# Optimization experiments

Measured on AMD Instinct MI355X. Metric: run time of the kernel, lower is better.

## Reference

```python
import jax, jax.numpy as jnp
import numpy as np

N_NODES = 50000
N_EDGES = 800000
N_GRAPHS = 512
IN_CH = 64
HID = 64
NEG_SLOPE = 0.2  # PyG GATConv default


def leaky_relu(x):
    return jnp.where(x >= 0, x, NEG_SLOPE * x)


def gat_conv(x, src, dst, W, a_src, a_dst, bias):
    # x: [N, in]; src/dst: [E] (self-loops already included)
    h = x @ W                                   # [N, hid]
    # per-edge attention logits (heads=1)
    alpha_s = h @ a_src                         # [N]
    alpha_d = h @ a_dst                         # [N]
    logits = leaky_relu(alpha_s[src] + alpha_d[dst])   # [E]
    # segment softmax over destination nodes
    seg_max = jax.ops.segment_max(logits, dst, num_segments=N_NODES)
    seg_max = jnp.where(jnp.isfinite(seg_max), seg_max, 0.0)
    ex = jnp.exp(logits - seg_max[dst])
    denom = jax.ops.segment_sum(ex, dst, num_segments=N_NODES)
    alpha = ex / jnp.maximum(denom[dst], 1e-16)
    # scatter-weighted aggregation of source features
    out = jax.ops.segment_sum(alpha[:, None] * h[src], dst, num_segments=N_NODES)
    return out + bias


def setup_inputs() -> dict:
    key = jax.random.key(0)
    ks = jax.random.split(key, 12)
    x = jax.random.normal(ks[0], (N_NODES, IN_CH), dtype=jnp.float32)
    edge_index = jax.random.randint(ks[1], (2, N_EDGES), 0, N_NODES, dtype=jnp.int64)
    batch = jnp.sort(jax.random.randint(ks[2], (N_NODES,), 0, N_GRAPHS, dtype=jnp.int64))
    s1 = 1.0 / np.sqrt(IN_CH)
    s2 = 1.0 / np.sqrt(HID)
    W1 = jax.random.normal(ks[3], (IN_CH, HID), dtype=jnp.float32) * s1
    a_src1 = jax.random.normal(ks[4], (HID,), dtype=jnp.float32) * s2
    a_dst1 = jax.random.normal(ks[5], (HID,), dtype=jnp.float32) * s2
    b1 = jnp.zeros((HID,), dtype=jnp.float32)
    W2 = jax.random.normal(ks[6], (HID, HID), dtype=jnp.float32) * s2
    a_src2 = jax.random.normal(ks[7], (HID,), dtype=jnp.float32) * s2
    a_dst2 = jax.random.normal(ks[8], (HID,), dtype=jnp.float32) * s2
    b2 = jnp.zeros((HID,), dtype=jnp.float32)
    return {"x": x, "edge_index": edge_index, "batch": batch,
            "W1": W1, "a_src1": a_src1, "a_dst1": a_dst1, "b1": b1,
            "W2": W2, "a_src2": a_src2, "a_dst2": a_dst2, "b2": b2}


def reference(x, edge_index, batch, W1, a_src1, a_dst1, b1, W2, a_src2, a_dst2, b2):
    # add self-loops (PyG GATConv default add_self_loops=True)
    loops = jnp.arange(N_NODES, dtype=edge_index.dtype)
    src = jnp.concatenate([edge_index[0], loops])
    dst = jnp.concatenate([edge_index[1], loops])
    h = jax.nn.elu(gat_conv(x, src, dst, W1, a_src1, a_dst1, b1))
    h = jax.nn.elu(gat_conv(h, src, dst, W2, a_src2, a_dst2, b2))
    # global mean pool per graph
    sums = jax.ops.segment_sum(h, batch, num_segments=N_GRAPHS)        # [G, hid]
    cnt = jax.ops.segment_sum(jnp.ones((N_NODES,), h.dtype), batch, num_segments=N_GRAPHS)
    return sums / jnp.maximum(cnt, 1.0)[:, None]
```

## Files before the change

### kernel.cpp

```cpp
#include <hip/hip_runtime.h>
#include <hip/hip_bf16.h>
#include <math.h>

#define N_NODES_C 50000
#define N_EDGES_C 800000
#define E_TOT_C   (N_EDGES_C + N_NODES_C)
#define N_GRAPHS_C 512
#define CH 64
#define NBUCK 391
#define NB_BUCK 256
#define BCAP 3328
#define TRF_NODES 64
#define NB_TRF ((N_NODES_C + TRF_NODES - 1) / TRF_NODES)

__device__ __forceinline__ float wave_reduce_sum(float v) {
#pragma unroll
    for (int m = 32; m >= 1; m >>= 1) v += __shfl_xor(v, m, 64);
    return v;
}


__global__ __launch_bounds__(256) void prelim_kernel(
    const int* __restrict__ batch, int* __restrict__ gstart, int* __restrict__ bucket_cnt,
    const float* __restrict__ W1, const float* __restrict__ as1, const float* __restrict__ ad1,
    const float* __restrict__ W2, const float* __restrict__ as2, const float* __restrict__ ad2,
    float* __restrict__ wa)
{
    int blk = blockIdx.x, t = threadIdx.x;
    if (blk >= 196) {
        if (t < 64) {
            const float* W  = (blk == 196) ? W1  : W2;
            const float* As = (blk == 196) ? as1 : as2;
            const float* Ad = (blk == 196) ? ad1 : ad2;
            float ss = 0.f, dd = 0.f;
#pragma unroll 8
            for (int c = 0; c < 64; ++c) {
                float w = W[t * 64 + c];
                ss = fmaf(w, As[c], ss);
                dd = fmaf(w, Ad[c], dd);
            }
            float* o = wa + ((blk == 196) ? 0 : 128);
            o[t] = ss; o[64 + t] = dd;
        }
        return;
    }
    int i = blk * 256 + t;
    if (i < NBUCK) bucket_cnt[i] = 0;
    if (i >= N_NODES_C) return;
    int bcur = batch[i];
    int bprev = (i > 0) ? batch[i - 1] : -1;
    for (int g = bprev + 1; g <= bcur; ++g) gstart[g] = i;
    if (i == N_NODES_C - 1)
        for (int g = bcur + 1; g <= N_GRAPHS_C; ++g) gstart[g] = N_NODES_C;
}


struct TrfSmem {
    float Wl[64][64];
    __align__(16) float xs[64][68];
    float wsv[64], wdv[64];
};
struct BuildSmem { int cnt[NBUCK]; int lbase[NBUCK]; };
union __align__(16) FusedSmem { TrfSmem t; BuildSmem b; };


__device__ __forceinline__ void build_body(
    BuildSmem& sm, int blk, const int* __restrict__ ei,
    int* __restrict__ bucket_cnt, unsigned int* __restrict__ buck_edges)
{
    int t = threadIdx.x;
    for (int i = t; i < NBUCK; i += 256) sm.cnt[i] = 0;
    __syncthreads();
    const int CHUNK = (E_TOT_C + NB_BUCK - 1) / NB_BUCK;
    int beg = blk * CHUNK, end = min(beg + CHUNK, E_TOT_C);
    for (int e = beg + t; e < end; e += 256) {
        int d = (e < N_EDGES_C) ? ei[N_EDGES_C + e] : (e - N_EDGES_C);
        atomicAdd(&sm.cnt[d >> 7], 1);
    }
    __syncthreads();
    for (int b = t; b < NBUCK; b += 256) {
        int c = sm.cnt[b];
        sm.lbase[b] = (c > 0) ? atomicAdd(&bucket_cnt[b], c) : 0;
        sm.cnt[b] = 0;
    }
    __syncthreads();
    for (int e = beg + t; e < end; e += 256) {
        int s_, d_;
        if (e < N_EDGES_C) { s_ = ei[e]; d_ = ei[N_EDGES_C + e]; }
        else               { s_ = d_ = e - N_EDGES_C; }
        int b = d_ >> 7;
        int pos = sm.lbase[b] + atomicAdd(&sm.cnt[b], 1);
        buck_edges[b * BCAP + pos] = ((unsigned)(d_ & 127) << 16) | (unsigned)s_;
    }
}


__device__ __forceinline__ void transform_body(
    TrfSmem& sm, int bb,
    const float* __restrict__ xin, const float* __restrict__ W,
    const float* __restrict__ wa,
    __hip_bfloat16* __restrict__ hout, float* __restrict__ as_out,
    float* __restrict__ ad_out)
{
    int t = threadIdx.x;
    const float4* W4 = (const float4*)W;
    float4* Wl4 = (float4*)&sm.Wl[0][0];
    for (int i = t; i < 1024; i += 256) Wl4[i] = W4[i];
    if (t < 64) sm.wsv[t] = wa[t];
    else if (t < 128) sm.wdv[t - 64] = wa[t];
    int n0 = bb * TRF_NODES;
    int nn = min(TRF_NODES, N_NODES_C - n0);
    if (nn < TRF_NODES) {
        for (int idx = t; idx < 64 * TRF_NODES; idx += 256) {
            int k = idx >> 6, row = idx & 63;
            if (row >= nn) sm.xs[k][row] = 0.f;
        }
    }
    for (int idx = t; idx < nn * 16; idx += 256) {
        int row = idx >> 4, f4 = idx & 15;
        float4 v = *reinterpret_cast<const float4*>(xin + (size_t)(n0 + row) * CH + f4 * 4);
        sm.xs[f4 * 4 + 0][row] = v.x;
        sm.xs[f4 * 4 + 1][row] = v.y;
        sm.xs[f4 * 4 + 2][row] = v.z;
        sm.xs[f4 * 4 + 3][row] = v.w;
    }
    __syncthreads();
    int w = t >> 6, c = t & 63, lane = t & 63;
    int r0 = w * 16;
    float acc[16];
#pragma unroll
    for (int i = 0; i < 16; ++i) acc[i] = 0.f;
#pragma unroll 8
    for (int k = 0; k < 64; ++k) {
        float wl = sm.Wl[k][c];
        const float4* xp = reinterpret_cast<const float4*>(&sm.xs[k][r0]);
        float4 xa = xp[0], xb = xp[1], xc = xp[2], xd = xp[3];
        acc[0]  = fmaf(xa.x, wl, acc[0]);  acc[1]  = fmaf(xa.y, wl, acc[1]);
        acc[2]  = fmaf(xa.z, wl, acc[2]);  acc[3]  = fmaf(xa.w, wl, acc[3]);
        acc[4]  = fmaf(xb.x, wl, acc[4]);  acc[5]  = fmaf(xb.y, wl, acc[5]);
        acc[6]  = fmaf(xb.z, wl, acc[6]);  acc[7]  = fmaf(xb.w, wl, acc[7]);
        acc[8]  = fmaf(xc.x, wl, acc[8]);  acc[9]  = fmaf(xc.y, wl, acc[9]);
        acc[10] = fmaf(xc.z, wl, acc[10]); acc[11] = fmaf(xc.w, wl, acc[11]);
        acc[12] = fmaf(xd.x, wl, acc[12]); acc[13] = fmaf(xd.y, wl, acc[13]);
        acc[14] = fmaf(xd.z, wl, acc[14]); acc[15] = fmaf(xd.w, wl, acc[15]);
    }
    size_t hb = (size_t)(n0 + r0) * CH + c;
#pragma unroll
    for (int i = 0; i < 16; ++i)
        if (r0 + i < nn) hout[hb + (size_t)i * CH] = __float2bfloat16(acc[i]);
    int kb = lane & 3;
    int rloc = r0 + (lane >> 2);
    float ps = 0.f, pd = 0.f;
#pragma unroll
    for (int j = 0; j < 16; ++j) {
        int k = kb + 4 * j;
        float xv = sm.xs[k][rloc];
        ps = fmaf(xv, sm.wsv[k], ps);
        pd = fmaf(xv, sm.wdv[k], pd);
    }
    ps += __shfl_xor(ps, 1, 64); ps += __shfl_xor(ps, 2, 64);
    pd += __shfl_xor(pd, 1, 64); pd += __shfl_xor(pd, 2, 64);
    if (kb == 0 && rloc < nn) {
        as_out[n0 + rloc] = ps;
        ad_out[n0 + rloc] = pd;
    }
}


__global__ __launch_bounds__(256) void fused_build_trf(
    const int* __restrict__ ei, int* __restrict__ bucket_cnt,
    unsigned int* __restrict__ buck_edges,
    const float* __restrict__ xin, const float* __restrict__ W,
    const float* __restrict__ wa,
    __hip_bfloat16* __restrict__ hout, float* __restrict__ as_out,
    float* __restrict__ ad_out)
{
    __shared__ FusedSmem sm;
    if (blockIdx.x < NB_BUCK)
        build_body(sm.b, blockIdx.x, ei, bucket_cnt, buck_edges);
    else
        transform_body(sm.t, blockIdx.x - NB_BUCK, xin, W, wa, hout, as_out, ad_out);
}

__global__ __launch_bounds__(256) void transform_kernel(
    const float* __restrict__ xin, const float* __restrict__ W,
    const float* __restrict__ wa,
    __hip_bfloat16* __restrict__ hout, float* __restrict__ as_out,
    float* __restrict__ ad_out)
{
    __shared__ TrfSmem sm;
    transform_body(sm, blockIdx.x, xin, W, wa, hout, as_out, ad_out);
}


__global__ __launch_bounds__(512) void bucket_to_csr(const unsigned int* __restrict__ buck_edges,
                                                     const int* __restrict__ bucket_cnt,
                                                     unsigned short* __restrict__ csr_src,
                                                     unsigned int* __restrict__ row_ptr) {
    __shared__ unsigned int ebuf[BCAP];
    __shared__ unsigned short sbuf[BCAP];
    __shared__ int deg[128], off[128], cur[128];
    __shared__ int wsum;
    int bb = blockIdx.x, t = threadIdx.x;
    int base = bb * BCAP;
    int size = min(bucket_cnt[bb], BCAP);
    int node0 = bb << 7;
    int nnodes = min(128, N_NODES_C - node0);
    for (int i = t; i < size; i += 512) ebuf[i] = buck_edges[base + i];
    if (t < 128) deg[t] = 0;
    __syncthreads();
    for (int i = t; i < size; i += 512) atomicAdd(&deg[(ebuf[i] >> 16) & 127], 1);
    __syncthreads();
    int myscan = 0;
    if (t < 128) {
        int l = t & 63;
        int s = deg[t];
#pragma unroll
        for (int o = 1; o < 64; o <<= 1) {
            int u = __shfl_up(s, o, 64);
            if (l >= o) s += u;
        }
        myscan = s;
        if (t == 63) wsum = s;
    }
    __syncthreads();
    if (t < 128) {
        int add = (t >= 64) ? wsum : 0;
        off[t] = myscan + add - deg[t];
        cur[t] = 0;
    }
    __syncthreads();
    for (int i = t; i < size; i += 512) {
        unsigned pk = ebuf[i];
        int l = (pk >> 16) & 127;
        int p = atomicAdd(&cur[l], 1);
        sbuf[off[l] + p] = (unsigned short)(pk & 0xFFFFu);
    }
    __syncthreads();
    for (int i = t; i < size; i += 512) csr_src[base + i] = sbuf[i];
    if (t < nnodes)
        row_ptr[node0 + t] = ((unsigned)(base + off[t]) << 8) | (unsigned)min(deg[t], 255);
}


__global__ __launch_bounds__(256) void aggregate_kernel(
    const __hip_bfloat16* __restrict__ h, const float* __restrict__ as,
    const float* __restrict__ ad, const float* __restrict__ bias,
    const unsigned int* __restrict__ row_ptr, const unsigned short* __restrict__ csr_src,
    float* __restrict__ out)
{
    int t = threadIdx.x;
    int w = t >> 6, lane = t & 63;
    int n = blockIdx.x * 4 + w;
    unsigned rp = row_ptr[n];
    int beg = (int)(rp >> 8);
    int deg = (int)(rp & 255u);
    float adn = ad[n];
    if (deg <= 64) {
        int sub = lane >> 3;
        int cg  = (lane & 7) << 3;
        int ch  = cg | sub;
        float bch = bias[ch];
        int s_reg = (int)csr_src[beg + min(lane, deg - 1)];
        float ex = 0.f;
        if (lane < deg) {
            float v = as[s_reg] + adn;
            v = (v >= 0.f) ? v : 0.2f * v;
            ex = __expf(v);
        }
        float ssum = wave_reduce_sum(ex);
        float inv = 1.f / fmaxf(ssum, 1e-16f);
        float a0 = 0.f, a1 = 0.f, a2 = 0.f, a3 = 0.f;
        float a4 = 0.f, a5 = 0.f, a6 = 0.f, a7 = 0.f;
        int full = deg >> 4, rem = deg & 15;
        for (int j = 0; j < full; ++j) {
            int e1 = j * 16 + sub;
            int e2 = e1 + 8;
            int   s1 = __shfl(s_reg, e1, 64);
            int   s2 = __shfl(s_reg, e2, 64);
            float w1 = __shfl(ex, e1, 64);
            float w2 = __shfl(ex, e2, 64);
            uint4 u1 = *reinterpret_cast<const uint4*>(h + (size_t)s1 * CH + cg);
            uint4 u2 = *reinterpret_cast<const uint4*>(h + (size_t)s2 * CH + cg);
            a0 = fmaf(w1, __uint_as_float(u1.x << 16), a0);
            a1 = fmaf(w1, __uint_as_float(u1.x & 0xFFFF0000u), a1);
            a2 = fmaf(w1, __uint_as_float(u1.y << 16), a2);
            a3 = fmaf(w1, __uint_as_float(u1.y & 0xFFFF0000u), a3);
            a4 = fmaf(w1, __uint_as_float(u1.z << 16), a4);
            a5 = fmaf(w1, __uint_as_float(u1.z & 0xFFFF0000u), a5);
            a6 = fmaf(w1, __uint_as_float(u1.w << 16), a6);
            a7 = fmaf(w1, __uint_as_float(u1.w & 0xFFFF0000u), a7);
            a0 = fmaf(w2, __uint_as_float(u2.x << 16), a0);
            a1 = fmaf(w2, __uint_as_float(u2.x & 0xFFFF0000u), a1);
            a2 = fmaf(w2, __uint_as_float(u2.y << 16), a2);
            a3 = fmaf(w2, __uint_as_float(u2.y & 0xFFFF0000u), a3);
            a4 = fmaf(w2, __uint_as_float(u2.z << 16), a4);
            a5 = fmaf(w2, __uint_as_float(u2.z & 0xFFFF0000u), a5);
            a6 = fmaf(w2, __uint_as_float(u2.w << 16), a6);
            a7 = fmaf(w2, __uint_as_float(u2.w & 0xFFFF0000u), a7);
        }
        if (rem) {
            int e1 = full * 16 + sub;
            int   s1 = __shfl(s_reg, e1, 64);
            float w1 = __shfl(ex, e1, 64);
            uint4 u1 = make_uint4(0, 0, 0, 0);
            if (e1 < deg) u1 = *reinterpret_cast<const uint4*>(h + (size_t)s1 * CH + cg);
            a0 = fmaf(w1, __uint_as_float(u1.x << 16), a0);
            a1 = fmaf(w1, __uint_as_float(u1.x & 0xFFFF0000u), a1);
            a2 = fmaf(w1, __uint_as_float(u1.y << 16), a2);
            a3 = fmaf(w1, __uint_as_float(u1.y & 0xFFFF0000u), a3);
            a4 = fmaf(w1, __uint_as_float(u1.z << 16), a4);
            a5 = fmaf(w1, __uint_as_float(u1.z & 0xFFFF0000u), a5);
            a6 = fmaf(w1, __uint_as_float(u1.w << 16), a6);
            a7 = fmaf(w1, __uint_as_float(u1.w & 0xFFFF0000u), a7);
            if (rem > 8) {
                int e2 = e1 + 8;
                int   s2 = __shfl(s_reg, e2, 64);
                float w2 = __shfl(ex, e2, 64);
                uint4 u2 = make_uint4(0, 0, 0, 0);
                if (e2 < deg) u2 = *reinterpret_cast<const uint4*>(h + (size_t)s2 * CH + cg);
                a0 = fmaf(w2, __uint_as_float(u2.x << 16), a0);
                a1 = fmaf(w2, __uint_as_float(u2.x & 0xFFFF0000u), a1);
                a2 = fmaf(w2, __uint_as_float(u2.y << 16), a2);
                a3 = fmaf(w2, __uint_as_float(u2.y & 0xFFFF0000u), a3);
                a4 = fmaf(w2, __uint_as_float(u2.z << 16), a4);
                a5 = fmaf(w2, __uint_as_float(u2.z & 0xFFFF0000u), a5);
                a6 = fmaf(w2, __uint_as_float(u2.w << 16), a6);
                a7 = fmaf(w2, __uint_as_float(u2.w & 0xFFFF0000u), a7);
            }
        }
        bool hi5 = (lane & 32) != 0;
        float t0 = __shfl_xor(hi5 ? a0 : a4, 32, 64);
        float t1 = __shfl_xor(hi5 ? a1 : a5, 32, 64);
        float t2 = __shfl_xor(hi5 ? a2 : a6, 32, 64);
        float t3 = __shfl_xor(hi5 ? a3 : a7, 32, 64);
        float b0 = (hi5 ? a4 : a0) + t0;
        float b1 = (hi5 ? a5 : a1) + t1;
        float b2 = (hi5 ? a6 : a2) + t2;
        float b3 = (hi5 ? a7 : a3) + t3;
        bool hi4 = (lane & 16) != 0;
        float u0 = __shfl_xor(hi4 ? b0 : b2, 16, 64);
        float u1s = __shfl_xor(hi4 ? b1 : b3, 16, 64);
        float c0 = (hi4 ? b2 : b0) + u0;
        float c1 = (hi4 ? b3 : b1) + u1s;
        bool hi3 = (lane & 8) != 0;
        float v1 = __shfl_xor(hi3 ? c0 : c1, 8, 64);
        float r  = (hi3 ? c1 : c0) + v1;
        float v = r * inv + bch;
        v = (v > 0.f) ? v : __expf(v) - 1.f;
        out[(size_t)n * CH + ch] = v;
    } else {
        int end = beg + deg;
        float ssum = 0.f;
        for (int i = beg + lane; i < end; i += 64) {
            float v = as[csr_src[i]] + adn;
            v = (v >= 0.f) ? v : 0.2f * v;
            ssum += __expf(v);
        }
        ssum = wave_reduce_sum(ssum);
        float inv = 1.f / fmaxf(ssum, 1e-16f);
        float acc = 0.f;
        for (int i = beg; i < end; ++i) {
            int s = csr_src[i];
            float v = as[s] + adn;
            v = (v >= 0.f) ? v : 0.2f * v;
            float ww = __expf(v);
            acc = fmaf(ww, __bfloat162float(h[(size_t)s * CH + lane]), acc);
        }
        acc = acc * inv + bias[lane];
        out[(size_t)n * CH + lane] = (acc > 0.f) ? acc : __expf(acc) - 1.f;
    }
}


__global__ __launch_bounds__(256) void pool_kernel(
    const float* __restrict__ h, const int* __restrict__ gstart,
    float* __restrict__ out)
{
    __shared__ float red[4][64];
    int g = blockIdx.x;
    int t = threadIdx.x, w = t >> 6, lane = t & 63;
    int beg = gstart[g], end = gstart[g + 1];
    float acc = 0.f;
    for (int n = beg + w; n < end; n += 4) acc += h[n * CH + lane];
    red[w][lane] = acc;
    __syncthreads();
    if (w == 0) {
        float v = red[0][lane] + red[1][lane] + red[2][lane] + red[3][lane];
        float c = (float)(end - beg);
        out[g * CH + lane] = v / fmaxf(c, 1.f);
    }
}


extern "C" void kernel_launch(void* const* d_in, const int* in_sizes, int n_in,
                              void* d_out, int out_size, void* d_ws, size_t ws_size,
                              hipStream_t stream)
{
    const float* x   = (const float*)d_in[0];
    const int*   ei  = (const int*)d_in[1];
    const int*   bat = (const int*)d_in[2];
    const float* W1  = (const float*)d_in[3];
    const float* as1 = (const float*)d_in[4];
    const float* ad1 = (const float*)d_in[5];
    const float* b1  = (const float*)d_in[6];
    const float* W2  = (const float*)d_in[7];
    const float* as2 = (const float*)d_in[8];
    const float* ad2 = (const float*)d_in[9];
    const float* b2  = (const float*)d_in[10];
    float* out = (float*)d_out;

    char* ws = (char*)d_ws;
    size_t off = 0;
    auto alloc = [&](size_t bytes) -> void* {
        void* p = ws + off;
        off += (bytes + 255) & ~size_t(255);
        return p;
    };
    __hip_bfloat16* hbuf = (__hip_bfloat16*)alloc(sizeof(__hip_bfloat16) * N_NODES_C * CH);
    float* obuf    = (float*)alloc(sizeof(float) * N_NODES_C * CH);
    float* alpha_s = (float*)alloc(sizeof(float) * N_NODES_C);
    float* alpha_d = (float*)alloc(sizeof(float) * N_NODES_C);
    int*   bucket_cnt = (int*)alloc(sizeof(int) * NBUCK);
    unsigned int* buck_edges = (unsigned int*)alloc(sizeof(unsigned) * NBUCK * BCAP);
    unsigned short* csr_src  = (unsigned short*)alloc(sizeof(unsigned short) * NBUCK * BCAP);
    unsigned int* row_ptr    = (unsigned int*)alloc(sizeof(unsigned) * N_NODES_C);
    int*   gstart  = (int*)alloc(sizeof(int) * (N_GRAPHS_C + 1));
    float* wa      = (float*)alloc(sizeof(float) * 256);

    const int NB_AGG = N_NODES_C / 4;

    prelim_kernel<<<198, 256, 0, stream>>>(bat, gstart, bucket_cnt,
                                           W1, as1, ad1, W2, as2, ad2, wa);
    fused_build_trf<<<NB_BUCK + NB_TRF, 256, 0, stream>>>(ei, bucket_cnt, buck_edges,
                                                          x, W1, wa, hbuf, alpha_s, alpha_d);
    bucket_to_csr<<<NBUCK, 512, 0, stream>>>(buck_edges, bucket_cnt, csr_src, row_ptr);

    aggregate_kernel<<<NB_AGG, 256, 0, stream>>>(hbuf, alpha_s, alpha_d, b1,
                                                 row_ptr, csr_src, obuf);
    transform_kernel<<<NB_TRF, 256, 0, stream>>>(obuf, W2, wa + 128, hbuf, alpha_s, alpha_d);
    aggregate_kernel<<<NB_AGG, 256, 0, stream>>>(hbuf, alpha_s, alpha_d, b2,
                                                 row_ptr, csr_src, obuf);

    pool_kernel<<<N_GRAPHS_C, 256, 0, stream>>>(obuf, gstart, out);
}
```

Measured before the change: 180.2 us.

## Remove prelim kernel, fold its work into other kernels, add small-degree aggregate path

Result: faster. 175.0 us (-2.9%).

```diff
diff --git a/kernel.cpp b/kernel.cpp
--- a/kernel.cpp
+++ b/kernel.cpp
@@ -19,44 +19,20 @@
     return v;
 }
 
-
-__global__ __launch_bounds__(256) void prelim_kernel(
-    const int* __restrict__ batch, int* __restrict__ gstart, int* __restrict__ bucket_cnt,
-    const float* __restrict__ W1, const float* __restrict__ as1, const float* __restrict__ ad1,
-    const float* __restrict__ W2, const float* __restrict__ as2, const float* __restrict__ ad2,
-    float* __restrict__ wa)
-{
-    int blk = blockIdx.x, t = threadIdx.x;
-    if (blk >= 196) {
-        if (t < 64) {
-            const float* W  = (blk == 196) ? W1  : W2;
-            const float* As = (blk == 196) ? as1 : as2;
-            const float* Ad = (blk == 196) ? ad1 : ad2;
-            float ss = 0.f, dd = 0.f;
-#pragma unroll 8
-            for (int c = 0; c < 64; ++c) {
-                float w = W[t * 64 + c];
-                ss = fmaf(w, As[c], ss);
-                dd = fmaf(w, Ad[c], dd);
-            }
-            float* o = wa + ((blk == 196) ? 0 : 128);
-            o[t] = ss; o[64 + t] = dd;
-        }
-        return;
-    }
-    int i = blk * 256 + t;
-    if (i < NBUCK) bucket_cnt[i] = 0;
-    if (i >= N_NODES_C) return;
-    int bcur = batch[i];
-    int bprev = (i > 0) ? batch[i - 1] : -1;
-    for (int g = bprev + 1; g <= bcur; ++g) gstart[g] = i;
-    if (i == N_NODES_C - 1)
-        for (int g = bcur + 1; g <= N_GRAPHS_C; ++g) gstart[g] = N_NODES_C;
-}
-
-
-struct TrfSmem {
-    float Wl[64][64];
+__device__ __forceinline__ void fma8(float wv, uint4 u, float* a) {
+    a[0] = fmaf(wv, __uint_as_float(u.x << 16), a[0]);
+    a[1] = fmaf(wv, __uint_as_float(u.x & 0xFFFF0000u), a[1]);
+    a[2] = fmaf(wv, __uint_as_float(u.y << 16), a[2]);
+    a[3] = fmaf(wv, __uint_as_float(u.y & 0xFFFF0000u), a[3]);
+    a[4] = fmaf(wv, __uint_as_float(u.z << 16), a[4]);
+    a[5] = fmaf(wv, __uint_as_float(u.z & 0xFFFF0000u), a[5]);
+    a[6] = fmaf(wv, __uint_as_float(u.w << 16), a[6]);
+    a[7] = fmaf(wv, __uint_as_float(u.w & 0xFFFF0000u), a[7]);
+}
+
+
+struct __align__(16) TrfSmem {
+    __align__(16) float Wl[64][68];
     __align__(16) float xs[64][68];
     float wsv[64], wdv[64];
 };
@@ -98,16 +74,16 @@
 __device__ __forceinline__ void transform_body(
     TrfSmem& sm, int bb,
     const float* __restrict__ xin, const float* __restrict__ W,
-    const float* __restrict__ wa,
+    const float* __restrict__ a_s, const float* __restrict__ a_d,
     __hip_bfloat16* __restrict__ hout, float* __restrict__ as_out,
     float* __restrict__ ad_out)
 {
     int t = threadIdx.x;
     const float4* W4 = (const float4*)W;
-    float4* Wl4 = (float4*)&sm.Wl[0][0];
-    for (int i = t; i < 1024; i += 256) Wl4[i] = W4[i];
-    if (t < 64) sm.wsv[t] = wa[t];
-    else if (t < 128) sm.wdv[t - 64] = wa[t];
+    for (int i = t; i < 1024; i += 256) {
+        int row = i >> 4, f4 = i & 15;
+        *reinterpret_cast<float4*>(&sm.Wl[row][f4 * 4]) = W4[i];
+    }
     int n0 = bb * TRF_NODES;
     int nn = min(TRF_NODES, N_NODES_C - n0);
     if (nn < TRF_NODES) {
@@ -125,6 +101,16 @@
         sm.xs[f4 * 4 + 3][row] = v.w;
     }
     __syncthreads();
+    if (t < 64) {
+        float ss = 0.f, dd = 0.f;
+#pragma unroll 8
+        for (int c2 = 0; c2 < 64; ++c2) {
+            float wv = sm.Wl[t][c2];
+            ss = fmaf(wv, a_s[c2], ss);
+            dd = fmaf(wv, a_d[c2], dd);
+        }
+        sm.wsv[t] = ss; sm.wdv[t] = dd;
+    }
     int w = t >> 6, c = t & 63, lane = t & 63;
     int r0 = w * 16;
     float acc[16];
@@ -148,6 +134,7 @@
 #pragma unroll
     for (int i = 0; i < 16; ++i)
         if (r0 + i < nn) hout[hb + (size_t)i * CH] = __float2bfloat16(acc[i]);
+    __syncthreads();
     int kb = lane & 3;
     int rloc = r0 + (lane >> 2);
     float ps = 0.f, pd = 0.f;
@@ -171,7 +158,7 @@
     const int* __restrict__ ei, int* __restrict__ bucket_cnt,
     unsigned int* __restrict__ buck_edges,
     const float* __restrict__ xin, const float* __restrict__ W,
-    const float* __restrict__ wa,
+    const float* __restrict__ a_s, const float* __restrict__ a_d,
     __hip_bfloat16* __restrict__ hout, float* __restrict__ as_out,
     float* __restrict__ ad_out)
 {
@@ -179,29 +166,41 @@
     if (blockIdx.x < NB_BUCK)
         build_body(sm.b, blockIdx.x, ei, bucket_cnt, buck_edges);
     else
-        transform_body(sm.t, blockIdx.x - NB_BUCK, xin, W, wa, hout, as_out, ad_out);
+        transform_body(sm.t, blockIdx.x - NB_BUCK, xin, W, a_s, a_d, hout, as_out, ad_out);
 }
 
 __global__ __launch_bounds__(256) void transform_kernel(
     const float* __restrict__ xin, const float* __restrict__ W,
-    const float* __restrict__ wa,
+    const float* __restrict__ a_s, const float* __restrict__ a_d,
     __hip_bfloat16* __restrict__ hout, float* __restrict__ as_out,
     float* __restrict__ ad_out)
 {
     __shared__ TrfSmem sm;
-    transform_body(sm, blockIdx.x, xin, W, wa, hout, as_out, ad_out);
+    transform_body(sm, blockIdx.x, xin, W, a_s, a_d, hout, as_out, ad_out);
 }
 
 
 __global__ __launch_bounds__(512) void bucket_to_csr(const unsigned int* __restrict__ buck_edges,
                                                      const int* __restrict__ bucket_cnt,
+                                                     const int* __restrict__ batch,
                                                      unsigned short* __restrict__ csr_src,
-                                                     unsigned int* __restrict__ row_ptr) {
+                                                     unsigned int* __restrict__ row_ptr,
+                                                     int* __restrict__ gstart) {
     __shared__ unsigned int ebuf[BCAP];
     __shared__ unsigned short sbuf[BCAP];
     __shared__ int deg[128], off[128], cur[128];
     __shared__ int wsum;
     int bb = blockIdx.x, t = threadIdx.x;
+    if (bb < 196 && t < 256) {
+        int i = bb * 256 + t;
+        if (i < N_NODES_C) {
+            int bcur = batch[i];
+            int bprev = (i > 0) ? batch[i - 1] : -1;
+            for (int g = bprev + 1; g <= bcur; ++g) gstart[g] = i;
+            if (i == N_NODES_C - 1)
+                for (int g = bcur + 1; g <= N_GRAPHS_C; ++g) gstart[g] = N_NODES_C;
+        }
+    }
     int base = bb * BCAP;
     int size = min(bucket_cnt[bb], BCAP);
     int node0 = bb << 7;
@@ -253,13 +252,64 @@
     int w = t >> 6, lane = t & 63;
     int n = blockIdx.x * 4 + w;
     unsigned rp = row_ptr[n];
+    float adn = ad[n];
     int beg = (int)(rp >> 8);
     int deg = (int)(rp & 255u);
-    float adn = ad[n];
-    if (deg <= 64) {
-        int sub = lane >> 3;
-        int cg  = (lane & 7) << 3;
-        int ch  = cg | sub;
+    int sub = lane >> 3;
+    int cg  = (lane & 7) << 3;
+    int ch  = cg | sub;
+    if (deg <= 32) {
+        float bch = bias[ch];
+        int dm = deg - 1;
+        int s_reg = (int)csr_src[beg + min(lane, dm)];
+        float asv = as[s_reg];
+        int e0 = sub, e1 = sub + 8;
+        int s0 = __shfl(s_reg, min(e0, dm), 64);
+        int s1 = __shfl(s_reg, min(e1, dm), 64);
+        uint4 u0 = *reinterpret_cast<const uint4*>(h + (size_t)s0 * CH + cg);
+        uint4 u1 = *reinterpret_cast<const uint4*>(h + (size_t)s1 * CH + cg);
+        bool two = (deg > 16);
+        int e2 = sub + 16, e3 = sub + 24;
+        uint4 u2 = make_uint4(0, 0, 0, 0), u3 = make_uint4(0, 0, 0, 0);
+        if (two) {
+            int s2 = __shfl(s_reg, min(e2, dm), 64);
+            int s3 = __shfl(s_reg, min(e3, dm), 64);
+            u2 = *reinterpret_cast<const uint4*>(h + (size_t)s2 * CH + cg);
+            u3 = *reinterpret_cast<const uint4*>(h + (size_t)s3 * CH + cg);
+        }
+        float v0 = asv + adn;
+        v0 = (v0 >= 0.f) ? v0 : 0.2f * v0;
+        float ex = (lane < deg) ? __expf(v0) : 0.f;
+        float w0 = __shfl(ex, e0, 64), w1 = __shfl(ex, e1, 64);
+        float ssum = wave_reduce_sum(ex);
+        float a[8] = {0.f, 0.f, 0.f, 0.f, 0.f, 0.f, 0.f, 0.f};
+        fma8(w0, u0, a); fma8(w1, u1, a);
+        if (two) {
+            float w2 = __shfl(ex, e2, 64), w3 = __shfl(ex, e3, 64);
+            fma8(w2, u2, a); fma8(w3, u3, a);
+        }
+        float inv = 1.f / fmaxf(ssum, 1e-16f);
+        bool hi5 = (lane & 32) != 0;
+        float t0 = __shfl_xor(hi5 ? a[0] : a[4], 32, 64);
+        float t1 = __shfl_xor(hi5 ? a[1] : a[5], 32, 64);
+        float t2 = __shfl_xor(hi5 ? a[2] : a[6], 32, 64);
+        float t3 = __shfl_xor(hi5 ? a[3] : a[7], 32, 64);
+        float b0 = (hi5 ? a[4] : a[0]) + t0;
+        float b1 = (hi5 ? a[5] : a[1]) + t1;
+        float b2 = (hi5 ? a[6] : a[2]) + t2;
+        float b3 = (hi5 ? a[7] : a[3]) + t3;
+        bool hi4 = (lane & 16) != 0;
+        float u0s = __shfl_xor(hi4 ? b0 : b2, 16, 64);
+        float u1s = __shfl_xor(hi4 ? b1 : b3, 16, 64);
+        float c0 = (hi4 ? b2 : b0) + u0s;
+        float c1 = (hi4 ? b3 : b1) + u1s;
+        bool hi3 = (lane & 8) != 0;
+        float v1 = __shfl_xor(hi3 ? c0 : c1, 8, 64);
+        float r  = (hi3 ? c1 : c0) + v1;
+        float v = r * inv + bch;
+        v = (v > 0.f) ? v : __expf(v) - 1.f;
+        out[(size_t)n * CH + ch] = v;
+    } else if (deg <= 64) {
         float bch = bias[ch];
         int s_reg = (int)csr_src[beg + min(lane, deg - 1)];
         float ex = 0.f;
@@ -270,8 +320,7 @@
         }
         float ssum = wave_reduce_sum(ex);
         float inv = 1.f / fmaxf(ssum, 1e-16f);
-        float a0 = 0.f, a1 = 0.f, a2 = 0.f, a3 = 0.f;
-        float a4 = 0.f, a5 = 0.f, a6 = 0.f, a7 = 0.f;
+        float a[8] = {0.f, 0.f, 0.f, 0.f, 0.f, 0.f, 0.f, 0.f};
         int full = deg >> 4, rem = deg & 15;
         for (int j = 0; j < full; ++j) {
             int e1 = j * 16 + sub;
@@ -282,66 +331,36 @@
             float w2 = __shfl(ex, e2, 64);
             uint4 u1 = *reinterpret_cast<const uint4*>(h + (size_t)s1 * CH + cg);
             uint4 u2 = *reinterpret_cast<const uint4*>(h + (size_t)s2 * CH + cg);
-            a0 = fmaf(w1, __uint_as_float(u1.x << 16), a0);
-            a1 = fmaf(w1, __uint_as_float(u1.x & 0xFFFF0000u), a1);
-            a2 = fmaf(w1, __uint_as_float(u1.y << 16), a2);
-            a3 = fmaf(w1, __uint_as_float(u1.y & 0xFFFF0000u), a3);
-            a4 = fmaf(w1, __uint_as_float(u1.z << 16), a4);
-            a5 = fmaf(w1, __uint_as_float(u1.z & 0xFFFF0000u), a5);
-            a6 = fmaf(w1, __uint_as_float(u1.w << 16), a6);
-            a7 = fmaf(w1, __uint_as_float(u1.w & 0xFFFF0000u), a7);
-            a0 = fmaf(w2, __uint_as_float(u2.x << 16), a0);
-            a1 = fmaf(w2, __uint_as_float(u2.x & 0xFFFF0000u), a1);
-            a2 = fmaf(w2, __uint_as_float(u2.y << 16), a2);
-            a3 = fmaf(w2, __uint_as_float(u2.y & 0xFFFF0000u), a3);
-            a4 = fmaf(w2, __uint_as_float(u2.z << 16), a4);
-            a5 = fmaf(w2, __uint_as_float(u2.z & 0xFFFF0000u), a5);
-            a6 = fmaf(w2, __uint_as_float(u2.w << 16), a6);
-            a7 = fmaf(w2, __uint_as_float(u2.w & 0xFFFF0000u), a7);
+            fma8(w1, u1, a); fma8(w2, u2, a);
         }
         if (rem) {
+            int dm = deg - 1;
             int e1 = full * 16 + sub;
-            int   s1 = __shfl(s_reg, e1, 64);
+            int   s1 = __shfl(s_reg, min(e1, dm), 64);
             float w1 = __shfl(ex, e1, 64);
-            uint4 u1 = make_uint4(0, 0, 0, 0);
-            if (e1 < deg) u1 = *reinterpret_cast<const uint4*>(h + (size_t)s1 * CH + cg);
-            a0 = fmaf(w1, __uint_as_float(u1.x << 16), a0);
-            a1 = fmaf(w1, __uint_as_float(u1.x & 0xFFFF0000u), a1);
-            a2 = fmaf(w1, __uint_as_float(u1.y << 16), a2);
-            a3 = fmaf(w1, __uint_as_float(u1.y & 0xFFFF0000u), a3);
-            a4 = fmaf(w1, __uint_as_float(u1.z << 16), a4);
-            a5 = fmaf(w1, __uint_as_float(u1.z & 0xFFFF0000u), a5);
-            a6 = fmaf(w1, __uint_as_float(u1.w << 16), a6);
-            a7 = fmaf(w1, __uint_as_float(u1.w & 0xFFFF0000u), a7);
+            uint4 u1 = *reinterpret_cast<const uint4*>(h + (size_t)s1 * CH + cg);
+            fma8(w1, u1, a);
             if (rem > 8) {
                 int e2 = e1 + 8;
-                int   s2 = __shfl(s_reg, e2, 64);
+                int   s2 = __shfl(s_reg, min(e2, dm), 64);
                 float w2 = __shfl(ex, e2, 64);
-                uint4 u2 = make_uint4(0, 0, 0, 0);
-                if (e2 < deg) u2 = *reinterpret_cast<const uint4*>(h + (size_t)s2 * CH + cg);
-                a0 = fmaf(w2, __uint_as_float(u2.x << 16), a0);
-                a1 = fmaf(w2, __uint_as_float(u2.x & 0xFFFF0000u), a1);
-                a2 = fmaf(w2, __uint_as_float(u2.y << 16), a2);
-                a3 = fmaf(w2, __uint_as_float(u2.y & 0xFFFF0000u), a3);
-                a4 = fmaf(w2, __uint_as_float(u2.z << 16), a4);
-                a5 = fmaf(w2, __uint_as_float(u2.z & 0xFFFF0000u), a5);
-                a6 = fmaf(w2, __uint_as_float(u2.w << 16), a6);
-                a7 = fmaf(w2, __uint_as_float(u2.w & 0xFFFF0000u), a7);
+                uint4 u2 = *reinterpret_cast<const uint4*>(h + (size_t)s2 * CH + cg);
+                fma8(w2, u2, a);
             }
         }
         bool hi5 = (lane & 32) != 0;
-        float t0 = __shfl_xor(hi5 ? a0 : a4, 32, 64);
-        float t1 = __shfl_xor(hi5 ? a1 : a5, 32, 64);
-        float t2 = __shfl_xor(hi5 ? a2 : a6, 32, 64);
-        float t3 = __shfl_xor(hi5 ? a3 : a7, 32, 64);
-        float b0 = (hi5 ? a4 : a0) + t0;
-        float b1 = (hi5 ? a5 : a1) + t1;
-        float b2 = (hi5 ? a6 : a2) + t2;
-        float b3 = (hi5 ? a7 : a3) + t3;
+        float t0 = __shfl_xor(hi5 ? a[0] : a[4], 32, 64);
+        float t1 = __shfl_xor(hi5 ? a[1] : a[5], 32, 64);
+        float t2 = __shfl_xor(hi5 ? a[2] : a[6], 32, 64);
+        float t3 = __shfl_xor(hi5 ? a[3] : a[7], 32, 64);
+        float b0 = (hi5 ? a[4] : a[0]) + t0;
+        float b1 = (hi5 ? a[5] : a[1]) + t1;
+        float b2 = (hi5 ? a[6] : a[2]) + t2;
+        float b3 = (hi5 ? a[7] : a[3]) + t3;
         bool hi4 = (lane & 16) != 0;
-        float u0 = __shfl_xor(hi4 ? b0 : b2, 16, 64);
+        float u0s = __shfl_xor(hi4 ? b0 : b2, 16, 64);
         float u1s = __shfl_xor(hi4 ? b1 : b3, 16, 64);
-        float c0 = (hi4 ? b2 : b0) + u0;
+        float c0 = (hi4 ? b2 : b0) + u0s;
         float c1 = (hi4 ? b3 : b1) + u1s;
         bool hi3 = (lane & 8) != 0;
         float v1 = __shfl_xor(hi3 ? c0 : c1, 8, 64);
@@ -426,19 +445,19 @@
     unsigned short* csr_src  = (unsigned short*)alloc(sizeof(unsigned short) * NBUCK * BCAP);
     unsigned int* row_ptr    = (unsigned int*)alloc(sizeof(unsigned) * N_NODES_C);
     int*   gstart  = (int*)alloc(sizeof(int) * (N_GRAPHS_C + 1));
-    float* wa      = (float*)alloc(sizeof(float) * 256);
 
     const int NB_AGG = N_NODES_C / 4;
 
-    prelim_kernel<<<198, 256, 0, stream>>>(bat, gstart, bucket_cnt,
-                                           W1, as1, ad1, W2, as2, ad2, wa);
+    hipMemsetAsync(bucket_cnt, 0, sizeof(int) * NBUCK, stream);
     fused_build_trf<<<NB_BUCK + NB_TRF, 256, 0, stream>>>(ei, bucket_cnt, buck_edges,
-                                                          x, W1, wa, hbuf, alpha_s, alpha_d);
-    bucket_to_csr<<<NBUCK, 512, 0, stream>>>(buck_edges, bucket_cnt, csr_src, row_ptr);
+                                                          x, W1, as1, ad1,
+                                                          hbuf, alpha_s, alpha_d);
+    bucket_to_csr<<<NBUCK, 512, 0, stream>>>(buck_edges, bucket_cnt, bat,
+                                             csr_src, row_ptr, gstart);
 
     aggregate_kernel<<<NB_AGG, 256, 0, stream>>>(hbuf, alpha_s, alpha_d, b1,
                                                  row_ptr, csr_src, obuf);
-    transform_kernel<<<NB_TRF, 256, 0, stream>>>(obuf, W2, wa + 128, hbuf, alpha_s, alpha_d);
+    transform_kernel<<<NB_TRF, 256, 0, stream>>>(obuf, W2, as2, ad2, hbuf, alpha_s, alpha_d);
     aggregate_kernel<<<NB_AGG, 256, 0, stream>>>(hbuf, alpha_s, alpha_d, b2,
                                                  row_ptr, csr_src, obuf);
 
```
